# Performance work log

Hardware: AMD Instinct MI355X
Metric: run time of the kernel (lower is better)

Reference implementation:

```python
import jax, jax.numpy as jnp
import numpy as np

N = 10000; E = 320000; NFEAT = 128; NHID = 128; NOUT = 1; C0 = 10; C1 = 5


def setup_inputs() -> dict:
    key = jax.random.key(0)
    ks = jax.random.split(key, 20)
    p = lambda i, sh: jax.random.normal(ks[i], sh, jnp.float32) * 0.05
    u0 = jax.random.uniform(ks[2], (N, C0), jnp.float32, 1e-6, 1.0 - 1e-6)
    u1 = jax.random.uniform(ks[3], (C0, C1), jnp.float32, 1e-6, 1.0 - 1e-6)
    return dict(
        x=jax.random.normal(ks[0], (N, NFEAT), jnp.float32),
        edge_weight=jax.random.uniform(ks[1], (E,), jnp.float32),
        gumbel0=-jnp.log(-jnp.log(u0)),
        gumbel1=-jnp.log(-jnp.log(u1)),
        conv1_w=p(4, (NFEAT, NHID)), conv1_b=jnp.zeros(NHID, jnp.float32),
        conv2_w=p(5, (NHID, NHID)), conv2_b=jnp.zeros(NHID, jnp.float32),
        bn1_g=jnp.ones(NHID, jnp.float32), bn1_b=jnp.zeros(NHID, jnp.float32),
        bn2_g=jnp.ones(NHID, jnp.float32), bn2_b=jnp.zeros(NHID, jnp.float32),
        enc1_w=p(6, (NFEAT + 2 * NHID, NHID)), enc1_b=jnp.zeros(NHID, jnp.float32),
        enc2_w=p(7, (NHID, NHID)), enc2_b=jnp.zeros(NHID, jnp.float32),
        ml0_w=p(8, (NHID, C0)), ml0_b=jnp.zeros(C0, jnp.float32),
        ml1_w=p(9, (NHID, C1)), ml1_b=jnp.zeros(C1, jnp.float32),
        me0_w=p(10, (NHID, NHID)), me0_b=jnp.zeros(NHID, jnp.float32),
        me1_w=p(11, (NHID, NHID)), me1_b=jnp.zeros(NHID, jnp.float32),
        fc1_w=p(12, (3 * NHID, 512)), fc1_b=jnp.zeros(512, jnp.float32),
        fc2_w=p(13, (512, NOUT)), fc2_b=jnp.zeros(NOUT, jnp.float32),
        edge_index=jax.random.randint(ks[14], (2, E), 0, N),
    )


def _gcn(x, w, b, row, col, ew):
    # PyG GCNConv: add self loops (weight 1), sym norm D^-1/2 (A+I) D^-1/2
    h = x @ w
    deg = jax.ops.segment_sum(ew, col, num_segments=N) + 1.0
    dinv = jax.lax.rsqrt(deg)
    norm = dinv[row] * ew * dinv[col]
    agg = jax.ops.segment_sum(norm[:, None] * h[row], col, num_segments=N)
    return agg + h * (dinv * dinv)[:, None] + b


def _bn(x, g, b):
    m = x.mean(0)
    v = ((x - m) ** 2).mean(0)
    return (x - m) * jax.lax.rsqrt(v + 1e-5) * g + b


def _gumbel_hard(logits, g):
    # tau=1, hard=True straight-through gumbel softmax over dim=1
    y = jax.nn.softmax(logits + g, axis=1)
    hard = jax.nn.one_hot(jnp.argmax(y, axis=1), y.shape[1], dtype=y.dtype)
    return hard + y - jax.lax.stop_gradient(y)


def _l2rows(x):
    n = jnp.sqrt(jnp.sum(x * x, axis=1, keepdims=True))
    return x / jnp.maximum(n, 1e-12)


def _forward(edge_index, x, edge_weight, gumbel0, gumbel1,
             conv1_w, conv1_b, conv2_w, conv2_b, bn1_g, bn1_b, bn2_g, bn2_b,
             enc1_w, enc1_b, enc2_w, enc2_b, ml0_w, ml0_b, ml1_w, ml1_b,
             me0_w, me0_b, me1_w, me1_b, fc1_w, fc1_b, fc2_w, fc2_b):
    relu = jax.nn.relu
    row, col = edge_index[0], edge_index[1]
    # MPNN_Encoder (dropout = identity, BN uses batch stats as in training fwd)
    h1 = _bn(relu(_gcn(x, conv1_w, conv1_b, row, col, edge_weight)), bn1_g, bn1_b)
    h2 = _bn(relu(_gcn(h1, conv2_w, conv2_b, row, col, edge_weight)), bn2_g, bn2_b)
    cat = jnp.concatenate([x, h1, h2], axis=1)
    bottom = relu(relu(cat @ enc1_w + enc1_b) @ enc2_w + enc2_b)  # [N, NHID]
    # dense adjacency (adj.to_dense(); coalesce sums duplicate edges)
    adj = jnp.zeros((N, N), jnp.float32).at[row, col].add(edge_weight)
    latent = bottom
    product = None
    exts = []
    levels = [(ml0_w, ml0_b, me0_w, me0_b, gumbel0), (ml1_w, ml1_b, me1_w, me1_b, gumbel1)]
    for mlw, mlb, mew, meb, g in levels:
        assign = _gumbel_hard(latent @ mlw + mlb, g)          # [n_prev, C]
        product = assign if product is None else product @ assign  # [N, C]
        xp = _l2rows(assign.T @ latent)                        # [C, NHID]
        adj = assign.T @ adj @ assign                          # [C, C]
        adj = adj / jnp.sum(adj)
        latent = jnp.tanh((adj @ xp) @ mew + meb)              # [C, NHID]
        exts.append(product @ latent)                          # [N, NHID]
    rep = jnp.concatenate([bottom] + exts, axis=1)             # [N, 3*NHID]
    out = relu(relu(rep @ fc1_w + fc1_b) @ fc2_w + fc2_b)
    return out.reshape(-1)


def reference(x, edge_weight, gumbel0, gumbel1, conv1_w, conv1_b, conv2_w,
              conv2_b, bn1_g, bn1_b, bn2_g, bn2_b, enc1_w, enc1_b, enc2_w,
              enc2_b, ml0_w, ml0_b, ml1_w, ml1_b, me0_w, me0_b, me1_w, me1_b,
              fc1_w, fc1_b, fc2_w, fc2_b, edge_index):
    return _forward(edge_index, x, edge_weight, gumbel0, gumbel1,
                    conv1_w, conv1_b, conv2_w, conv2_b, bn1_g, bn1_b, bn2_g,
                    bn2_b, enc1_w, enc1_b, enc2_w, enc2_b, ml0_w, ml0_b,
                    ml1_w, ml1_b, me0_w, me0_b, me1_w, me1_b, fc1_w, fc1_b,
                    fc2_w, fc2_b)
```

## Files before the change

kernel.cpp:

```cpp
#include <hip/hip_runtime.h>

#define NN 10000
#define NE 320000
#define NH 128
#define C0N 10
#define C1N 5

__global__ void k_deg_cnt(const int* __restrict__ ei, const float* __restrict__ ew,
                          float* deg, int* cnt) {
  int e = blockIdx.x * 256 + threadIdx.x;
  if (e >= NE) return;
  int c = ei[NE + e];
  atomicAdd(&deg[c], ew[e]);
  atomicAdd(&cnt[c], 1);
}

__global__ __launch_bounds__(1024) void k_scan(const int* __restrict__ cnt, int* __restrict__ rowptr) {
  __shared__ int part[1024];
  int t = threadIdx.x;
  const int chunk = (NN + 1023) / 1024;
  int base = t * chunk;
  int s = 0;
  for (int i = 0; i < chunk; i++) { int idx = base + i; if (idx < NN) s += cnt[idx]; }
  part[t] = s; __syncthreads();
  for (int off = 1; off < 1024; off <<= 1) {
    int v = (t >= off) ? part[t - off] : 0;
    __syncthreads();
    part[t] += v;
    __syncthreads();
  }
  int run = (t == 0) ? 0 : part[t - 1];
  for (int i = 0; i < chunk; i++) { int idx = base + i; if (idx < NN) { rowptr[idx] = run; run += cnt[idx]; } }
  if (t == 1023) rowptr[NN] = run;
}

__global__ void k_fill(const int* __restrict__ ei, const float* __restrict__ ew,
                       const float* __restrict__ deg, const int* __restrict__ rowptr,
                       int* __restrict__ fill, int* __restrict__ csrs, float* __restrict__ csrw) {
  int e = blockIdx.x * 256 + threadIdx.x;
  if (e >= NE) return;
  int r = ei[e], c = ei[NE + e];
  float nrm = rsqrtf(deg[r] + 1.0f) * ew[e] * rsqrtf(deg[c] + 1.0f);
  int pos = rowptr[c] + atomicAdd(&fill[c], 1);
  csrs[pos] = r;
  csrw[pos] = nrm;
}

template<int BIAS, int RELU>
__global__ __launch_bounds__(256) void gemm_k(
    const float* __restrict__ A, int lda,
    const float* __restrict__ B, int ldb,
    const float* __restrict__ bias,
    float* __restrict__ C, int ldc,
    int M, int K) {
  __shared__ __align__(16) float As[16][36];
  __shared__ __align__(16) float Bs[16][68];
  int bm = blockIdx.x * 32, bn = blockIdx.y * 64;
  int t = threadIdx.x;
  int tx = t & 15, ty = t >> 4;
  float acc[2][4];
  #pragma unroll
  for (int i = 0; i < 2; i++)
    #pragma unroll
    for (int j = 0; j < 4; j++) acc[i][j] = 0.f;

  for (int k0 = 0; k0 < K; k0 += 16) {
    if (t < 128) {
      int la_r = t >> 2, la_k = (t & 3) * 4;
      int ar = bm + la_r;
      float4 av = make_float4(0.f, 0.f, 0.f, 0.f);
      if (ar < M) av = *reinterpret_cast<const float4*>(&A[(size_t)ar * lda + k0 + la_k]);
      As[la_k + 0][la_r] = av.x; As[la_k + 1][la_r] = av.y;
      As[la_k + 2][la_r] = av.z; As[la_k + 3][la_r] = av.w;
    }
    {
      int lb_k = t >> 4, lb_n = (t & 15) * 4;
      *reinterpret_cast<float4*>(&Bs[lb_k][lb_n]) =
          *reinterpret_cast<const float4*>(&B[(size_t)(k0 + lb_k) * ldb + bn + lb_n]);
    }
    __syncthreads();
    #pragma unroll
    for (int k = 0; k < 16; k++) {
      float2 af = *reinterpret_cast<const float2*>(&As[k][ty * 2]);
      float4 bf = *reinterpret_cast<const float4*>(&Bs[k][tx * 4]);
      acc[0][0] = fmaf(af.x, bf.x, acc[0][0]); acc[0][1] = fmaf(af.x, bf.y, acc[0][1]);
      acc[0][2] = fmaf(af.x, bf.z, acc[0][2]); acc[0][3] = fmaf(af.x, bf.w, acc[0][3]);
      acc[1][0] = fmaf(af.y, bf.x, acc[1][0]); acc[1][1] = fmaf(af.y, bf.y, acc[1][1]);
      acc[1][2] = fmaf(af.y, bf.z, acc[1][2]); acc[1][3] = fmaf(af.y, bf.w, acc[1][3]);
    }
    __syncthreads();
  }
  int cb = bn + tx * 4;
  float4 bias4 = make_float4(0.f, 0.f, 0.f, 0.f);
  if (BIAS) bias4 = *reinterpret_cast<const float4*>(&bias[cb]);
  #pragma unroll
  for (int i = 0; i < 2; i++) {
    int r = bm + ty * 2 + i;
    if (r >= M) continue;
    float4 v = make_float4(acc[i][0], acc[i][1], acc[i][2], acc[i][3]);
    if (BIAS) { v.x += bias4.x; v.y += bias4.y; v.z += bias4.z; v.w += bias4.w; }
    if (RELU) {
      v.x = fmaxf(v.x, 0.f); v.y = fmaxf(v.y, 0.f);
      v.z = fmaxf(v.z, 0.f); v.w = fmaxf(v.w, 0.f);
    }
    *reinterpret_cast<float4*>(&C[(size_t)r * ldc + cb]) = v;
  }
}

__global__ __launch_bounds__(256) void gemm_bn(
    const float* __restrict__ A,
    const float* __restrict__ sums,
    const float* __restrict__ g, const float* __restrict__ b,
    const float* __restrict__ B,
    float* __restrict__ C, int M) {
  __shared__ __align__(16) float As[16][36];
  __shared__ __align__(16) float Bs[16][68];
  int bm = blockIdx.x * 32, bn = blockIdx.y * 64;
  int t = threadIdx.x;
  int tx = t & 15, ty = t >> 4;
  float acc[2][4];
  #pragma unroll
  for (int i = 0; i < 2; i++)
    #pragma unroll
    for (int j = 0; j < 4; j++) acc[i][j] = 0.f;

  const float invn = 1.0f / NN;
  for (int k0 = 0; k0 < NH; k0 += 16) {
    if (t < 128) {
      int la_r = t >> 2, la_k = (t & 3) * 4;
      int ar = bm + la_r;
      int cb = k0 + la_k;
      float4 av = make_float4(0.f, 0.f, 0.f, 0.f);
      if (ar < M) {
        float4 raw = *reinterpret_cast<const float4*>(&A[(size_t)ar * NH + cb]);
        float4 sm = *reinterpret_cast<const float4*>(&sums[cb]);
        float4 sq = *reinterpret_cast<const float4*>(&sums[NH + cb]);
        float4 gv = *reinterpret_cast<const float4*>(&g[cb]);
        float4 bv = *reinterpret_cast<const float4*>(&b[cb]);
        float m0 = sm.x * invn, m1 = sm.y * invn, m2 = sm.z * invn, m3 = sm.w * invn;
        av.x = (raw.x - m0) * (gv.x * rsqrtf(sq.x * invn - m0 * m0 + 1e-5f)) + bv.x;
        av.y = (raw.y - m1) * (gv.y * rsqrtf(sq.y * invn - m1 * m1 + 1e-5f)) + bv.y;
        av.z = (raw.z - m2) * (gv.z * rsqrtf(sq.z * invn - m2 * m2 + 1e-5f)) + bv.z;
        av.w = (raw.w - m3) * (gv.w * rsqrtf(sq.w * invn - m3 * m3 + 1e-5f)) + bv.w;
      }
      As[la_k + 0][la_r] = av.x; As[la_k + 1][la_r] = av.y;
      As[la_k + 2][la_r] = av.z; As[la_k + 3][la_r] = av.w;
    }
    {
      int lb_k = t >> 4, lb_n = (t & 15) * 4;
      *reinterpret_cast<float4*>(&Bs[lb_k][lb_n]) =
          *reinterpret_cast<const float4*>(&B[(size_t)(k0 + lb_k) * NH + bn + lb_n]);
    }
    __syncthreads();
    #pragma unroll
    for (int k = 0; k < 16; k++) {
      float2 af = *reinterpret_cast<const float2*>(&As[k][ty * 2]);
      float4 bf = *reinterpret_cast<const float4*>(&Bs[k][tx * 4]);
      acc[0][0] = fmaf(af.x, bf.x, acc[0][0]); acc[0][1] = fmaf(af.x, bf.y, acc[0][1]);
      acc[0][2] = fmaf(af.x, bf.z, acc[0][2]); acc[0][3] = fmaf(af.x, bf.w, acc[0][3]);
      acc[1][0] = fmaf(af.y, bf.x, acc[1][0]); acc[1][1] = fmaf(af.y, bf.y, acc[1][1]);
      acc[1][2] = fmaf(af.y, bf.z, acc[1][2]); acc[1][3] = fmaf(af.y, bf.w, acc[1][3]);
    }
    __syncthreads();
  }
  int cb = bn + tx * 4;
  #pragma unroll
  for (int i = 0; i < 2; i++) {
    int r = bm + ty * 2 + i;
    if (r >= M) continue;
    float4 v = make_float4(acc[i][0], acc[i][1], acc[i][2], acc[i][3]);
    *reinterpret_cast<float4*>(&C[(size_t)r * NH + cb]) = v;
  }
}

__global__ __launch_bounds__(256) void gemm_cat3(
    const float* __restrict__ x,
    const float* __restrict__ hagg1, const float* __restrict__ sumsA,
    const float* __restrict__ gA, const float* __restrict__ bA,
    const float* __restrict__ hagg2, const float* __restrict__ sumsB,
    const float* __restrict__ gB, const float* __restrict__ bB,
    const float* __restrict__ B, const float* __restrict__ bias,
    float* __restrict__ C, int M) {
  __shared__ __align__(16) float As[16][36];
  __shared__ __align__(16) float Bs[16][68];
  int bm = blockIdx.x * 32, bn = blockIdx.y * 64;
  int t = threadIdx.x;
  int tx = t & 15, ty = t >> 4;
  float acc[2][4];
  #pragma unroll
  for (int i = 0; i < 2; i++)
    #pragma unroll
    for (int j = 0; j < 4; j++) acc[i][j] = 0.f;

  const float invn = 1.0f / NN;
  for (int k0 = 0; k0 < 3 * NH; k0 += 16) {
    if (t < 128) {
      int la_r = t >> 2, la_k = (t & 3) * 4;
      int src = k0 >> 7;
      int lc = (k0 + la_k) & (NH - 1);
      int ar = bm + la_r;
      float4 av = make_float4(0.f, 0.f, 0.f, 0.f);
      if (ar < M) {
        if (src == 0) {
          av = *reinterpret_cast<const float4*>(&x[(size_t)ar * NH + lc]);
        } else {
          const float* hp = (src == 1) ? hagg1 : hagg2;
          const float* sp = (src == 1) ? sumsA : sumsB;
          const float* gp = (src == 1) ? gA : gB;
          const float* bp = (src == 1) ? bA : bB;
          float4 raw = *reinterpret_cast<const float4*>(&hp[(size_t)ar * NH + lc]);
          float4 sm = *reinterpret_cast<const float4*>(&sp[lc]);
          float4 sq = *reinterpret_cast<const float4*>(&sp[NH + lc]);
          float4 gv = *reinterpret_cast<const float4*>(&gp[lc]);
          float4 bv = *reinterpret_cast<const float4*>(&bp[lc]);
          float m0 = sm.x * invn, m1 = sm.y * invn, m2 = sm.z * invn, m3 = sm.w * invn;
          av.x = (raw.x - m0) * (gv.x * rsqrtf(sq.x * invn - m0 * m0 + 1e-5f)) + bv.x;
          av.y = (raw.y - m1) * (gv.y * rsqrtf(sq.y * invn - m1 * m1 + 1e-5f)) + bv.y;
          av.z = (raw.z - m2) * (gv.z * rsqrtf(sq.z * invn - m2 * m2 + 1e-5f)) + bv.z;
          av.w = (raw.w - m3) * (gv.w * rsqrtf(sq.w * invn - m3 * m3 + 1e-5f)) + bv.w;
        }
      }
      As[la_k + 0][la_r] = av.x; As[la_k + 1][la_r] = av.y;
      As[la_k + 2][la_r] = av.z; As[la_k + 3][la_r] = av.w;
    }
    {
      int lb_k = t >> 4, lb_n = (t & 15) * 4;
      *reinterpret_cast<float4*>(&Bs[lb_k][lb_n]) =
          *reinterpret_cast<const float4*>(&B[(size_t)(k0 + lb_k) * NH + bn + lb_n]);
    }
    __syncthreads();
    #pragma unroll
    for (int k = 0; k < 16; k++) {
      float2 af = *reinterpret_cast<const float2*>(&As[k][ty * 2]);
      float4 bf = *reinterpret_cast<const float4*>(&Bs[k][tx * 4]);
      acc[0][0] = fmaf(af.x, bf.x, acc[0][0]); acc[0][1] = fmaf(af.x, bf.y, acc[0][1]);
      acc[0][2] = fmaf(af.x, bf.z, acc[0][2]); acc[0][3] = fmaf(af.x, bf.w, acc[0][3]);
      acc[1][0] = fmaf(af.y, bf.x, acc[1][0]); acc[1][1] = fmaf(af.y, bf.y, acc[1][1]);
      acc[1][2] = fmaf(af.y, bf.z, acc[1][2]); acc[1][3] = fmaf(af.y, bf.w, acc[1][3]);
    }
    __syncthreads();
  }
  int cb = bn + tx * 4;
  float4 bias4 = *reinterpret_cast<const float4*>(&bias[cb]);
  #pragma unroll
  for (int i = 0; i < 2; i++) {
    int r = bm + ty * 2 + i;
    if (r >= M) continue;
    float4 v;
    v.x = fmaxf(acc[i][0] + bias4.x, 0.f);
    v.y = fmaxf(acc[i][1] + bias4.y, 0.f);
    v.z = fmaxf(acc[i][2] + bias4.z, 0.f);
    v.w = fmaxf(acc[i][3] + bias4.w, 0.f);
    *reinterpret_cast<float4*>(&C[(size_t)r * NH + cb]) = v;
  }
}

__global__ void k_aggregate(const float* __restrict__ hpre, const int* __restrict__ rowptr,
                            const int* __restrict__ src, const float* __restrict__ wgt,
                            const float* __restrict__ deg, const float* __restrict__ bias,
                            float* __restrict__ outp) {
  int node = blockIdx.x * 8 + (threadIdx.x >> 5);
  int lane = threadIdx.x & 31;
  if (node >= NN) return;
  const float4* h4 = reinterpret_cast<const float4*>(hpre);
  int beg = rowptr[node], end = rowptr[node + 1];
  float4 a = make_float4(0.f, 0.f, 0.f, 0.f);
  for (int e = beg; e < end; e++) {
    int s = src[e]; float w = wgt[e];
    float4 hv = h4[(size_t)s * 32 + lane];
    a.x = fmaf(w, hv.x, a.x); a.y = fmaf(w, hv.y, a.y);
    a.z = fmaf(w, hv.z, a.z); a.w = fmaf(w, hv.w, a.w);
  }
  float d2 = 1.0f / (deg[node] + 1.0f);
  float4 hn = h4[(size_t)node * 32 + lane];
  float4 bv = reinterpret_cast<const float4*>(bias)[lane];
  float4 o;
  o.x = fmaxf(fmaf(hn.x, d2, a.x) + bv.x, 0.f);
  o.y = fmaxf(fmaf(hn.y, d2, a.y) + bv.y, 0.f);
  o.z = fmaxf(fmaf(hn.z, d2, a.z) + bv.z, 0.f);
  o.w = fmaxf(fmaf(hn.w, d2, a.w) + bv.w, 0.f);
  reinterpret_cast<float4*>(outp)[(size_t)node * 32 + lane] = o;
}

__global__ void k_bnstats(const float* __restrict__ x, float* __restrict__ sums) {
  int f = threadIdx.x;
  int rows_per = (NN + gridDim.x - 1) / gridDim.x;
  int r0 = blockIdx.x * rows_per, r1 = min(NN, r0 + rows_per);
  float s = 0.f, ss = 0.f;
  for (int r = r0; r < r1; r++) {
    float v = x[(size_t)r * NH + f];
    s += v; ss = fmaf(v, v, ss);
  }
  atomicAdd(&sums[f], s);
  atomicAdd(&sums[NH + f], ss);
}

__global__ __launch_bounds__(128) void k_assign_xp0(
    const float* __restrict__ bottom, const float* __restrict__ mlw,
    const float* __restrict__ mlb, const float* __restrict__ gum,
    int* __restrict__ c0g, float* __restrict__ xp) {
  __shared__ float accs[C0N][NH];
  __shared__ float ws[NH * C0N];
  __shared__ int c0s[128];
  int f = threadIdx.x;
  for (int i = f; i < NH * C0N; i += 128) ws[i] = mlw[i];
  #pragma unroll
  for (int c = 0; c < C0N; c++) accs[c][f] = 0.f;
  int r0 = blockIdx.x * 128;
  int node = r0 + f;
  __syncthreads();
  if (node < NN) {
    float a[C0N];
    #pragma unroll
    for (int c = 0; c < C0N; c++) a[c] = mlb[c] + gum[node * C0N + c];
    for (int k = 0; k < NH; k += 4) {
      float4 xv = *reinterpret_cast<const float4*>(&bottom[(size_t)node * NH + k]);
      #pragma unroll
      for (int c = 0; c < C0N; c++) {
        a[c] = fmaf(xv.x, ws[(k + 0) * C0N + c], a[c]);
        a[c] = fmaf(xv.y, ws[(k + 1) * C0N + c], a[c]);
        a[c] = fmaf(xv.z, ws[(k + 2) * C0N + c], a[c]);
        a[c] = fmaf(xv.w, ws[(k + 3) * C0N + c], a[c]);
      }
    }
    int best = 0; float bv = a[0];
    #pragma unroll
    for (int c = 1; c < C0N; c++) if (a[c] > bv) { bv = a[c]; best = c; }
    c0s[f] = best; c0g[node] = best;
  }
  __syncthreads();
  int r1 = min(NN, r0 + 128);
  for (int r = r0; r < r1; r++)
    accs[c0s[r - r0]][f] += bottom[(size_t)r * NH + f];
  #pragma unroll
  for (int c = 0; c < C0N; c++) atomicAdd(&xp[c * NH + f], accs[c][f]);
}

__global__ void k_adj2(const int* __restrict__ ei, const float* __restrict__ ew,
                       const int* __restrict__ c0, float* __restrict__ adj2) {
  __shared__ float acc[C0N * C0N];
  int t = threadIdx.x;
  if (t < C0N * C0N) acc[t] = 0.f;
  __syncthreads();
  for (int e = blockIdx.x * blockDim.x + t; e < NE; e += gridDim.x * blockDim.x) {
    int a = c0[ei[e]], b = c0[ei[NE + e]];
    atomicAdd(&acc[a * C0N + b], ew[e]);
  }
  __syncthreads();
  if (t < C0N * C0N) atomicAdd(&adj2[t], acc[t]);
}

__global__ __launch_bounds__(128) void k_level01(
    const float* __restrict__ xp_in, const float* __restrict__ adj_in,
    const float* __restrict__ me0w, const float* __restrict__ me0b,
    const float* __restrict__ ml1w, const float* __restrict__ ml1b,
    const float* __restrict__ gum1,
    const float* __restrict__ me1w, const float* __restrict__ me1b,
    float* __restrict__ lat0g, int* __restrict__ m01g, float* __restrict__ lat1g) {
  __shared__ float xp[C0N][NH];
  __shared__ float ts[C0N][NH];
  __shared__ float lat[C0N][NH];
  __shared__ float adjn[C0N * C0N];
  __shared__ float red[NH];
  __shared__ float xp1[C1N][NH];
  __shared__ float t1[C1N][NH];
  __shared__ int   m01s[C0N];
  __shared__ float a3[C1N * C1N];
  int f = threadIdx.x;
  for (int c = 0; c < C0N; c++) xp[c][f] = xp_in[c * NH + f];
  red[f] = (f < C0N * C0N) ? adj_in[f] : 0.f;
  __syncthreads();
  for (int s = 64; s > 0; s >>= 1) { if (f < s) red[f] += red[f + s]; __syncthreads(); }
  float tot = red[0];
  __syncthreads();
  if (f < C0N * C0N) adjn[f] = adj_in[f] / tot;
  for (int c = 0; c < C0N; c++) {
    red[f] = xp[c][f] * xp[c][f];
    __syncthreads();
    for (int s = 64; s > 0; s >>= 1) { if (f < s) red[f] += red[f + s]; __syncthreads(); }
    float nrm = fmaxf(sqrtf(red[0]), 1e-12f);
    __syncthreads();
    xp[c][f] /= nrm;
  }
  __syncthreads();
  for (int i = 0; i < C0N; i++) {
    float a = 0.f;
    #pragma unroll
    for (int j = 0; j < C0N; j++) a = fmaf(adjn[i * C0N + j], xp[j][f], a);
    ts[i][f] = a;
  }
  __syncthreads();
  for (int i = 0; i < C0N; i++) {
    float a = me0b[f];
    for (int k = 0; k < NH; k++) a = fmaf(ts[i][k], me0w[k * NH + f], a);
    float l = tanhf(a);
    lat[i][f] = l;
    lat0g[i * NH + f] = l;
  }
  __syncthreads();
  if (f < C0N) {
    float best = -1e30f; int bi = 0;
    for (int c = 0; c < C1N; c++) {
      float a = ml1b[c] + gum1[f * C1N + c];
      for (int k = 0; k < NH; k++) a = fmaf(lat[f][k], ml1w[k * C1N + c], a);
      if (a > best) { best = a; bi = c; }
    }
    m01s[f] = bi; m01g[f] = bi;
  }
  if (f < C1N * C1N) a3[f] = 0.f;
  __syncthreads();
  #pragma unroll
  for (int a = 0; a < C1N; a++) xp1[a][f] = 0.f;
  for (int i = 0; i < C0N; i++) xp1[m01s[i]][f] += lat[i][f];
  for (int c = 0; c < C1N; c++) {
    red[f] = xp1[c][f] * xp1[c][f];
    __syncthreads();
    for (int s = 64; s > 0; s >>= 1) { if (f < s) red[f] += red[f + s]; __syncthreads(); }
    float nrm = fmaxf(sqrtf(red[0]), 1e-12f);
    __syncthreads();
    xp1[c][f] /= nrm;
  }
  if (f < C0N * C0N) atomicAdd(&a3[m01s[f / C0N] * C1N + m01s[f % C0N]], adjn[f]);
  __syncthreads();
  red[f] = (f < C1N * C1N) ? a3[f] : 0.f;
  __syncthreads();
  for (int s = 64; s > 0; s >>= 1) { if (f < s) red[f] += red[f + s]; __syncthreads(); }
  float tot1 = red[0];
  __syncthreads();
  for (int i = 0; i < C1N; i++) {
    float a = 0.f;
    #pragma unroll
    for (int j = 0; j < C1N; j++) a = fmaf(a3[i * C1N + j] / tot1, xp1[j][f], a);
    t1[i][f] = a;
  }
  __syncthreads();
  for (int i = 0; i < C1N; i++) {
    float a = me1b[f];
    for (int k = 0; k < NH; k++) a = fmaf(t1[i][k], me1w[k * NH + f], a);
    lat1g[i * NH + f] = tanhf(a);
  }
}

__global__ __launch_bounds__(256) void k_fc12(
    const float* __restrict__ bottom, const int* __restrict__ c0,
    const int* __restrict__ m01, const float* __restrict__ lat0,
    const float* __restrict__ lat1,
    const float* __restrict__ w1, const float* __restrict__ b1,
    const float* __restrict__ w2, const float* __restrict__ b2,
    float* __restrict__ out) {
  __shared__ float rs[16][384];
  __shared__ float wred[16][4];
  __shared__ int cc[16], mm[16];
  int t = threadIdx.x;
  int node0 = blockIdx.x * 16;
  if (t < 16) { int c = c0[node0 + t]; cc[t] = c; mm[t] = m01[c]; }
  __syncthreads();
  for (int i = t; i < 16 * 32; i += 256) {
    int m = i >> 5, k4 = i & 31;
    ((float4*)&rs[m][0])[k4]        = ((const float4*)&bottom[(size_t)(node0 + m) * NH])[k4];
    ((float4*)&rs[m][NH])[k4]       = ((const float4*)&lat0[cc[m] * NH])[k4];
    ((float4*)&rs[m][2 * NH])[k4]   = ((const float4*)&lat1[mm[m] * NH])[k4];
  }
  __syncthreads();
  float acc0[16], acc1[16];
  #pragma unroll
  for (int m = 0; m < 16; m++) { acc0[m] = 0.f; acc1[m] = 0.f; }
  for (int k = 0; k < 384; k += 4) {
    float wa0 = w1[(size_t)(k + 0) * 512 + t], wb0 = w1[(size_t)(k + 0) * 512 + t + 256];
    float wa1 = w1[(size_t)(k + 1) * 512 + t], wb1 = w1[(size_t)(k + 1) * 512 + t + 256];
    float wa2 = w1[(size_t)(k + 2) * 512 + t], wb2 = w1[(size_t)(k + 2) * 512 + t + 256];
    float wa3 = w1[(size_t)(k + 3) * 512 + t], wb3 = w1[(size_t)(k + 3) * 512 + t + 256];
    #pragma unroll
    for (int m = 0; m < 16; m++) {
      float4 r4 = *reinterpret_cast<const float4*>(&rs[m][k]);
      acc0[m] = fmaf(r4.x, wa0, acc0[m]); acc0[m] = fmaf(r4.y, wa1, acc0[m]);
      acc0[m] = fmaf(r4.z, wa2, acc0[m]); acc0[m] = fmaf(r4.w, wa3, acc0[m]);
      acc1[m] = fmaf(r4.x, wb0, acc1[m]); acc1[m] = fmaf(r4.y, wb1, acc1[m]);
      acc1[m] = fmaf(r4.z, wb2, acc1[m]); acc1[m] = fmaf(r4.w, wb3, acc1[m]);
    }
  }
  float b1a = b1[t], b1b = b1[t + 256];
  float w2a = w2[t], w2b = w2[t + 256];
  int lane = t & 63, wid = t >> 6;
  #pragma unroll
  for (int m = 0; m < 16; m++) {
    float v = fmaxf(acc0[m] + b1a, 0.f) * w2a + fmaxf(acc1[m] + b1b, 0.f) * w2b;
    #pragma unroll
    for (int off = 32; off; off >>= 1) v += __shfl_down(v, off, 64);
    if (lane == 0) wred[m][wid] = v;
  }
  __syncthreads();
  if (t < 16) {
    float s = wred[t][0] + wred[t][1] + wred[t][2] + wred[t][3];
    out[node0 + t] = fmaxf(s + b2[0], 0.f);
  }
}

extern "C" void kernel_launch(void* const* d_in, const int* in_sizes, int n_in,
                              void* d_out, int out_size, void* d_ws, size_t ws_size,
                              hipStream_t stream) {
  const float* x    = (const float*)d_in[0];
  const float* ew   = (const float*)d_in[1];
  const float* gum0 = (const float*)d_in[2];
  const float* gum1 = (const float*)d_in[3];
  const float* c1w  = (const float*)d_in[4];
  const float* c1b  = (const float*)d_in[5];
  const float* c2w  = (const float*)d_in[6];
  const float* c2b  = (const float*)d_in[7];
  const float* bn1g = (const float*)d_in[8];
  const float* bn1b = (const float*)d_in[9];
  const float* bn2g = (const float*)d_in[10];
  const float* bn2b = (const float*)d_in[11];
  const float* e1w  = (const float*)d_in[12];
  const float* e1b  = (const float*)d_in[13];
  const float* e2w  = (const float*)d_in[14];
  const float* e2b  = (const float*)d_in[15];
  const float* ml0w = (const float*)d_in[16];
  const float* ml0b = (const float*)d_in[17];
  const float* ml1w = (const float*)d_in[18];
  const float* ml1b = (const float*)d_in[19];
  const float* me0w = (const float*)d_in[20];
  const float* me0b = (const float*)d_in[21];
  const float* me1w = (const float*)d_in[22];
  const float* me1b = (const float*)d_in[23];
  const float* f1w  = (const float*)d_in[24];
  const float* f1b  = (const float*)d_in[25];
  const float* f2w  = (const float*)d_in[26];
  const float* f2b  = (const float*)d_in[27];
  const int*   eidx = (const int*)d_in[28];
  float* out = (float*)d_out;

  char* p = (char*)d_ws;
  auto carve = [&](size_t bytes) -> void* {
    void* r = (void*)p; p += (bytes + 255) & ~(size_t)255; return r;
  };
  char*  zbase  = p;
  float* deg    = (float*)carve(NN * 4);
  int*   cnt    = (int*)carve(NN * 4);
  int*   fill   = (int*)carve(NN * 4);
  float* bnA    = (float*)carve(256 * 4);
  float* bnB    = (float*)carve(256 * 4);
  float* xp0    = (float*)carve(C0N * NH * 4);
  float* adj2   = (float*)carve(C0N * C0N * 4);
  size_t zbytes = (size_t)(p - zbase);
  int*   rowptr = (int*)carve((NN + 1) * 4);
  int*   csrs   = (int*)carve((size_t)NE * 4);
  float* csrw   = (float*)carve((size_t)NE * 4);
  float* hpre   = (float*)carve((size_t)NN * NH * 4);
  float* hagg1  = (float*)carve((size_t)NN * NH * 4);
  float* hagg2  = (float*)carve((size_t)NN * NH * 4);
  int*   c0     = (int*)carve(NN * 4);
  float* lat0   = (float*)carve(C0N * NH * 4);
  int*   m01    = (int*)carve(C0N * 4);
  float* lat1   = (float*)carve(C1N * NH * 4);
  float* ench   = hpre;
  float* bottom = hagg1;

  hipMemsetAsync(zbase, 0, zbytes, stream);

  k_deg_cnt<<<(NE + 255) / 256, 256, 0, stream>>>(eidx, ew, deg, cnt);
  k_scan<<<1, 1024, 0, stream>>>(cnt, rowptr);

  dim3 gg((NN + 31) / 32, NH / 64);
  gemm_k<0, 0><<<gg, 256, 0, stream>>>(x, NH, c1w, NH, nullptr, hpre, NH, NN, NH);
  k_fill<<<(NE + 255) / 256, 256, 0, stream>>>(eidx, ew, deg, rowptr, fill, csrs, csrw);
  k_aggregate<<<(NN + 7) / 8, 256, 0, stream>>>(hpre, rowptr, csrs, csrw, deg, c1b, hagg1);
  k_bnstats<<<80, 128, 0, stream>>>(hagg1, bnA);
  gemm_bn<<<gg, 256, 0, stream>>>(hagg1, bnA, bn1g, bn1b, c2w, hpre, NN);
  k_aggregate<<<(NN + 7) / 8, 256, 0, stream>>>(hpre, rowptr, csrs, csrw, deg, c2b, hagg2);
  k_bnstats<<<80, 128, 0, stream>>>(hagg2, bnB);
  gemm_cat3<<<gg, 256, 0, stream>>>(x, hagg1, bnA, bn1g, bn1b,
                                    hagg2, bnB, bn2g, bn2b,
                                    e1w, e1b, ench, NN);
  gemm_k<1, 1><<<gg, 256, 0, stream>>>(ench, NH, e2w, NH, e2b, bottom, NH, NN, NH);
  k_assign_xp0<<<(NN + 127) / 128, 128, 0, stream>>>(bottom, ml0w, ml0b, gum0, c0, xp0);
  k_adj2<<<320, 256, 0, stream>>>(eidx, ew, c0, adj2);
  k_level01<<<1, 128, 0, stream>>>(xp0, adj2, me0w, me0b, ml1w, ml1b, gum1,
                                   me1w, me1b, lat0, m01, lat1);
  k_fc12<<<NN / 16, 256, 0, stream>>>(bottom, c0, m01, lat0, lat1,
                                      f1w, f1b, f2w, f2b, out);
}
```

Baseline: 520.0 us.

## Fuse BN statistics into aggregation, vectorize fc12, restructure level01 matvecs

The BN column sum and sum-of-squares are now accumulated inside the aggregation kernel through a shared-memory block reduction and atomics. This removes the two separate bnstats passes that re-read the full hidden matrices. The k_level01 matvecs are reordered so each weight is loaded once per k and applied to all cluster rows, which shortens the serial single-block chain. k_fc12 now uses 128-thread blocks of 8 nodes with float4 weight loads and 4 outputs per thread, at the cost of more atomics in the aggregation and more blocks re-reading fc1 weights.

```diff
diff --git a/kernel.cpp b/kernel.cpp
--- a/kernel.cpp
+++ b/kernel.cpp
@@ -258,10 +258,12 @@
 __global__ void k_aggregate(const float* __restrict__ hpre, const int* __restrict__ rowptr,
                             const int* __restrict__ src, const float* __restrict__ wgt,
                             const float* __restrict__ deg, const float* __restrict__ bias,
-                            float* __restrict__ outp) {
-  int node = blockIdx.x * 8 + (threadIdx.x >> 5);
-  int lane = threadIdx.x & 31;
-  if (node >= NN) return;
+                            float* __restrict__ outp, float* __restrict__ sums) {
+  __shared__ float bs8[8][32][4];
+  __shared__ float bq8[8][32][4];
+  int t = threadIdx.x;
+  int grp = t >> 5, lane = t & 31;
+  int node = blockIdx.x * 8 + grp;
   const float4* h4 = reinterpret_cast<const float4*>(hpre);
   int beg = rowptr[node], end = rowptr[node + 1];
   float4 a = make_float4(0.f, 0.f, 0.f, 0.f);
@@ -280,19 +282,19 @@
   o.z = fmaxf(fmaf(hn.z, d2, a.z) + bv.z, 0.f);
   o.w = fmaxf(fmaf(hn.w, d2, a.w) + bv.w, 0.f);
   reinterpret_cast<float4*>(outp)[(size_t)node * 32 + lane] = o;
-}
-
-__global__ void k_bnstats(const float* __restrict__ x, float* __restrict__ sums) {
-  int f = threadIdx.x;
-  int rows_per = (NN + gridDim.x - 1) / gridDim.x;
-  int r0 = blockIdx.x * rows_per, r1 = min(NN, r0 + rows_per);
-  float s = 0.f, ss = 0.f;
-  for (int r = r0; r < r1; r++) {
-    float v = x[(size_t)r * NH + f];
-    s += v; ss = fmaf(v, v, ss);
-  }
-  atomicAdd(&sums[f], s);
-  atomicAdd(&sums[NH + f], ss);
+  bs8[grp][lane][0] = o.x; bs8[grp][lane][1] = o.y;
+  bs8[grp][lane][2] = o.z; bs8[grp][lane][3] = o.w;
+  bq8[grp][lane][0] = o.x * o.x; bq8[grp][lane][1] = o.y * o.y;
+  bq8[grp][lane][2] = o.z * o.z; bq8[grp][lane][3] = o.w * o.w;
+  __syncthreads();
+  if (t < NH) {
+    int fl = t >> 2, fj = t & 3;
+    float s = 0.f, q = 0.f;
+    #pragma unroll
+    for (int g = 0; g < 8; g++) { s += bs8[g][fl][fj]; q += bq8[g][fl][fj]; }
+    atomicAdd(&sums[t], s);
+    atomicAdd(&sums[NH + t], q);
+  }
 }
 
 __global__ __launch_bounds__(128) void k_assign_xp0(
@@ -363,7 +365,7 @@
   __shared__ float adjn[C0N * C0N];
   __shared__ float red[NH];
   __shared__ float xp1[C1N][NH];
-  __shared__ float t1[C1N][NH];
+  __shared__ float t1s[C1N][NH];
   __shared__ int   m01s[C0N];
   __shared__ float a3[C1N * C1N];
   int f = threadIdx.x;
@@ -390,12 +392,21 @@
     ts[i][f] = a;
   }
   __syncthreads();
-  for (int i = 0; i < C0N; i++) {
-    float a = me0b[f];
-    for (int k = 0; k < NH; k++) a = fmaf(ts[i][k], me0w[k * NH + f], a);
-    float l = tanhf(a);
-    lat[i][f] = l;
-    lat0g[i * NH + f] = l;
+  {
+    float acc0[C0N];
+    #pragma unroll
+    for (int i = 0; i < C0N; i++) acc0[i] = 0.f;
+    for (int k = 0; k < NH; k++) {
+      float w = me0w[k * NH + f];
+      #pragma unroll
+      for (int i = 0; i < C0N; i++) acc0[i] = fmaf(ts[i][k], w, acc0[i]);
+    }
+    float b0 = me0b[f];
+    for (int i = 0; i < C0N; i++) {
+      float l = tanhf(acc0[i] + b0);
+      lat[i][f] = l;
+      lat0g[i * NH + f] = l;
+    }
   }
   __syncthreads();
   if (f < C0N) {
@@ -431,69 +442,85 @@
     float a = 0.f;
     #pragma unroll
     for (int j = 0; j < C1N; j++) a = fmaf(a3[i * C1N + j] / tot1, xp1[j][f], a);
-    t1[i][f] = a;
-  }
-  __syncthreads();
-  for (int i = 0; i < C1N; i++) {
-    float a = me1b[f];
-    for (int k = 0; k < NH; k++) a = fmaf(t1[i][k], me1w[k * NH + f], a);
-    lat1g[i * NH + f] = tanhf(a);
-  }
-}
-
-__global__ __launch_bounds__(256) void k_fc12(
+    t1s[i][f] = a;
+  }
+  __syncthreads();
+  {
+    float acc1[C1N];
+    #pragma unroll
+    for (int i = 0; i < C1N; i++) acc1[i] = 0.f;
+    for (int k = 0; k < NH; k++) {
+      float w = me1w[k * NH + f];
+      #pragma unroll
+      for (int i = 0; i < C1N; i++) acc1[i] = fmaf(t1s[i][k], w, acc1[i]);
+    }
+    float b1v = me1b[f];
+    for (int i = 0; i < C1N; i++) lat1g[i * NH + f] = tanhf(acc1[i] + b1v);
+  }
+}
+
+__device__ __forceinline__ float4 fma4(float s, float4 w, float4 a) {
+  a.x = fmaf(s, w.x, a.x); a.y = fmaf(s, w.y, a.y);
+  a.z = fmaf(s, w.z, a.z); a.w = fmaf(s, w.w, a.w);
+  return a;
+}
+
+__global__ __launch_bounds__(128) void k_fc12(
     const float* __restrict__ bottom, const int* __restrict__ c0,
     const int* __restrict__ m01, const float* __restrict__ lat0,
     const float* __restrict__ lat1,
     const float* __restrict__ w1, const float* __restrict__ b1,
     const float* __restrict__ w2, const float* __restrict__ b2,
     float* __restrict__ out) {
-  __shared__ float rs[16][384];
-  __shared__ float wred[16][4];
-  __shared__ int cc[16], mm[16];
+  __shared__ float rs[8][384];
+  __shared__ float wred[8][2];
+  __shared__ int cc[8], mm[8];
   int t = threadIdx.x;
-  int node0 = blockIdx.x * 16;
-  if (t < 16) { int c = c0[node0 + t]; cc[t] = c; mm[t] = m01[c]; }
-  __syncthreads();
-  for (int i = t; i < 16 * 32; i += 256) {
-    int m = i >> 5, k4 = i & 31;
-    ((float4*)&rs[m][0])[k4]        = ((const float4*)&bottom[(size_t)(node0 + m) * NH])[k4];
-    ((float4*)&rs[m][NH])[k4]       = ((const float4*)&lat0[cc[m] * NH])[k4];
-    ((float4*)&rs[m][2 * NH])[k4]   = ((const float4*)&lat1[mm[m] * NH])[k4];
-  }
-  __syncthreads();
-  float acc0[16], acc1[16];
-  #pragma unroll
-  for (int m = 0; m < 16; m++) { acc0[m] = 0.f; acc1[m] = 0.f; }
+  int node0 = blockIdx.x * 8;
+  if (t < 8) { int c = c0[node0 + t]; cc[t] = c; mm[t] = m01[c]; }
+  __syncthreads();
+  for (int i = t; i < 8 * 96; i += 128) {
+    int m = i / 96, k4 = i % 96;
+    float4 v;
+    if (k4 < 32)      v = ((const float4*)&bottom[(size_t)(node0 + m) * NH])[k4];
+    else if (k4 < 64) v = ((const float4*)&lat0[cc[m] * NH])[k4 - 32];
+    else              v = ((const float4*)&lat1[mm[m] * NH])[k4 - 64];
+    ((float4*)&rs[m][0])[k4] = v;
+  }
+  __syncthreads();
+  float4 acc[8];
+  #pragma unroll
+  for (int m = 0; m < 8; m++) acc[m] = make_float4(0.f, 0.f, 0.f, 0.f);
+  int h = 4 * t;
   for (int k = 0; k < 384; k += 4) {
-    float wa0 = w1[(size_t)(k + 0) * 512 + t], wb0 = w1[(size_t)(k + 0) * 512 + t + 256];
-    float wa1 = w1[(size_t)(k + 1) * 512 + t], wb1 = w1[(size_t)(k + 1) * 512 + t + 256];
-    float wa2 = w1[(size_t)(k + 2) * 512 + t], wb2 = w1[(size_t)(k + 2) * 512 + t + 256];
-    float wa3 = w1[(size_t)(k + 3) * 512 + t], wb3 = w1[(size_t)(k + 3) * 512 + t + 256];
-    #pragma unroll
-    for (int m = 0; m < 16; m++) {
-      float4 r4 = *reinterpret_cast<const float4*>(&rs[m][k]);
-      acc0[m] = fmaf(r4.x, wa0, acc0[m]); acc0[m] = fmaf(r4.y, wa1, acc0[m]);
-      acc0[m] = fmaf(r4.z, wa2, acc0[m]); acc0[m] = fmaf(r4.w, wa3, acc0[m]);
-      acc1[m] = fmaf(r4.x, wb0, acc1[m]); acc1[m] = fmaf(r4.y, wb1, acc1[m]);
-      acc1[m] = fmaf(r4.z, wb2, acc1[m]); acc1[m] = fmaf(r4.w, wb3, acc1[m]);
-    }
-  }
-  float b1a = b1[t], b1b = b1[t + 256];
-  float w2a = w2[t], w2b = w2[t + 256];
+    float4 w0 = *(const float4*)&w1[(size_t)(k + 0) * 512 + h];
+    float4 wv1 = *(const float4*)&w1[(size_t)(k + 1) * 512 + h];
+    float4 wv2 = *(const float4*)&w1[(size_t)(k + 2) * 512 + h];
+    float4 wv3 = *(const float4*)&w1[(size_t)(k + 3) * 512 + h];
+    #pragma unroll
+    for (int m = 0; m < 8; m++) {
+      float4 r = *(const float4*)&rs[m][k];
+      acc[m] = fma4(r.x, w0, acc[m]);
+      acc[m] = fma4(r.y, wv1, acc[m]);
+      acc[m] = fma4(r.z, wv2, acc[m]);
+      acc[m] = fma4(r.w, wv3, acc[m]);
+    }
+  }
+  float4 b14 = *(const float4*)&b1[h];
+  float4 w24 = *(const float4*)&w2[h];
   int lane = t & 63, wid = t >> 6;
   #pragma unroll
-  for (int m = 0; m < 16; m++) {
-    float v = fmaxf(acc0[m] + b1a, 0.f) * w2a + fmaxf(acc1[m] + b1b, 0.f) * w2b;
+  for (int m = 0; m < 8; m++) {
+    float v = fmaxf(acc[m].x + b14.x, 0.f) * w24.x
+            + fmaxf(acc[m].y + b14.y, 0.f) * w24.y
+            + fmaxf(acc[m].z + b14.z, 0.f) * w24.z
+            + fmaxf(acc[m].w + b14.w, 0.f) * w24.w;
     #pragma unroll
     for (int off = 32; off; off >>= 1) v += __shfl_down(v, off, 64);
     if (lane == 0) wred[m][wid] = v;
   }
   __syncthreads();
-  if (t < 16) {
-    float s = wred[t][0] + wred[t][1] + wred[t][2] + wred[t][3];
-    out[node0 + t] = fmaxf(s + b2[0], 0.f);
-  }
+  if (t < 8) out[node0 + t] = fmaxf(wred[t][0] + wred[t][1] + b2[0], 0.f);
 }
 
 extern "C" void kernel_launch(void* const* d_in, const int* in_sizes, int n_in,
@@ -564,11 +591,9 @@
   dim3 gg((NN + 31) / 32, NH / 64);
   gemm_k<0, 0><<<gg, 256, 0, stream>>>(x, NH, c1w, NH, nullptr, hpre, NH, NN, NH);
   k_fill<<<(NE + 255) / 256, 256, 0, stream>>>(eidx, ew, deg, rowptr, fill, csrs, csrw);
-  k_aggregate<<<(NN + 7) / 8, 256, 0, stream>>>(hpre, rowptr, csrs, csrw, deg, c1b, hagg1);
-  k_bnstats<<<80, 128, 0, stream>>>(hagg1, bnA);
+  k_aggregate<<<NN / 8, 256, 0, stream>>>(hpre, rowptr, csrs, csrw, deg, c1b, hagg1, bnA);
   gemm_bn<<<gg, 256, 0, stream>>>(hagg1, bnA, bn1g, bn1b, c2w, hpre, NN);
-  k_aggregate<<<(NN + 7) / 8, 256, 0, stream>>>(hpre, rowptr, csrs, csrw, deg, c2b, hagg2);
-  k_bnstats<<<80, 128, 0, stream>>>(hagg2, bnB);
+  k_aggregate<<<NN / 8, 256, 0, stream>>>(hpre, rowptr, csrs, csrw, deg, c2b, hagg2, bnB);
   gemm_cat3<<<gg, 256, 0, stream>>>(x, hagg1, bnA, bn1g, bn1b,
                                     hagg2, bnB, bn2g, bn2b,
                                     e1w, e1b, ench, NN);
@@ -577,6 +602,6 @@
   k_adj2<<<320, 256, 0, stream>>>(eidx, ew, c0, adj2);
   k_level01<<<1, 128, 0, stream>>>(xp0, adj2, me0w, me0b, ml1w, ml1b, gum1,
                                    me1w, me1b, lat0, m01, lat1);
-  k_fc12<<<NN / 16, 256, 0, stream>>>(bottom, c0, m01, lat0, lat1,
-                                      f1w, f1b, f2w, f2b, out);
-}
+  k_fc12<<<NN / 8, 128, 0, stream>>>(bottom, c0, m01, lat0, lat1,
+                                     f1w, f1b, f2w, f2b, out);
+}
```

Result: faster. 495.1 us (-4.8%).
